# Performance work log

Hardware: AMD Instinct MI355X
Metric: run time of the kernel (lower is better)

## Reference

```python
import jax, jax.numpy as jnp
import numpy as np

EMBED_DIM = 768
N_HEADS = 12
HEAD_DIM = EMBED_DIM // N_HEADS


def setup_inputs() -> dict:
    key = jax.random.key(0)
    ks = jax.random.split(key, 5)
    s = 1.0 / np.sqrt(EMBED_DIM)
    x = jax.random.normal(ks[0], (8, 1024, EMBED_DIM), dtype=jnp.float32)
    w_qkv = jax.random.normal(ks[1], (EMBED_DIM, 3 * EMBED_DIM), dtype=jnp.float32) * s
    b_qkv = jnp.zeros((3 * EMBED_DIM,), dtype=jnp.float32)
    w_proj = jax.random.normal(ks[2], (EMBED_DIM, EMBED_DIM), dtype=jnp.float32) * s
    b_proj = jnp.zeros((EMBED_DIM,), dtype=jnp.float32)
    return {"x": x, "w_qkv": w_qkv, "b_qkv": b_qkv, "w_proj": w_proj, "b_proj": b_proj}


def reference(x, w_qkv, b_qkv, w_proj, b_proj):
    B, S, D = x.shape
    H, Hd = N_HEADS, HEAD_DIM
    qkv = x @ w_qkv + b_qkv                      # [B,S,3D]
    qkv = qkv.reshape(B, S, 3, H, Hd).transpose(2, 0, 3, 1, 4)  # [3,B,H,S,Hd]
    q, k, v = qkv[0], qkv[1], qkv[2]
    scale = Hd ** -0.5
    attn = jnp.einsum('bhqd,bhkd->bhqk', q, k) * scale  # [B,H,S,S]
    attn = jax.nn.softmax(attn, axis=-1)
    out = jnp.einsum('bhqk,bhkd->bhqd', attn, v)        # [B,H,S,Hd]
    out = out.transpose(0, 2, 1, 3).reshape(B, S, D)
    return out @ w_proj + b_proj
```

## Files before the change

kernel.cpp:

```cpp
#include <hip/hip_runtime.h>
#include <stdint.h>

typedef unsigned short ushort_t;
typedef __bf16 bf16x8 __attribute__((ext_vector_type(8)));
typedef float floatx4 __attribute__((ext_vector_type(4)));

#define B_   8
#define S_   1024
#define D_   768
#define H_   12
#define M_   (B_ * S_)
#define N3_  (3 * D_)
#define QK_  1536

static __device__ __forceinline__ void gl_lds16(const void* g, void* l) {
  __builtin_amdgcn_global_load_lds((const __attribute__((address_space(1))) void*)g,
                                   (__attribute__((address_space(3))) void*)l,
                                   16, 0, 0);
}

static __device__ __forceinline__ ushort_t f2bf(float f) {
  __bf16 h = (__bf16)f;
  return __builtin_bit_cast(unsigned short, h);
}

static __device__ __forceinline__ void store_out(ushort_t* p, float v) { *p = f2bf(v); }
static __device__ __forceinline__ void store_out(float* p, float v) { *p = v; }

static __device__ __forceinline__ void transpose_tile(const float* __restrict__ W,
                                                      ushort_t* __restrict__ Wt,
                                                      int K, int N, int bx, int by,
                                                      int t) {
  __shared__ float tile[32][33];
  const int n0 = bx * 32, k0 = by * 32;
  const int tx = t & 31, ty = t >> 5;
#pragma unroll
  for (int i = 0; i < 4; ++i)
    tile[ty + i * 8][tx] = W[(size_t)(k0 + ty + i * 8) * N + n0 + tx];
  __syncthreads();
#pragma unroll
  for (int i = 0; i < 4; ++i)
    Wt[(size_t)(n0 + ty + i * 8) * K + k0 + tx] = f2bf(tile[tx][ty + i * 8]);
}

__global__ __launch_bounds__(256) void prep_kernel(const float* __restrict__ x,
                                                   ushort_t* __restrict__ xb,
                                                   const float* __restrict__ w_qkv,
                                                   ushort_t* __restrict__ wqkvt,
                                                   const float* __restrict__ w_proj,
                                                   ushort_t* __restrict__ wprojt) {
  const int gb = blockIdx.x, t = threadIdx.x;
  if (gb < 24576) {
    const int i = gb * 256 + t;
    xb[i] = f2bf(x[i]);
  } else if (gb < 24576 + 1728) {
    const int lb = gb - 24576;
    transpose_tile(w_qkv, wqkvt, D_, N3_, lb % 72, lb / 72, t);
  } else {
    const int lb = gb - 24576 - 1728;
    transpose_tile(w_proj, wprojt, D_, D_, lb % 24, lb / 24, t);
  }
}

template <typename OutT, bool SPLITV>
__global__ __launch_bounds__(256, 4) void gemm128(const ushort_t* __restrict__ A,
                                                  const ushort_t* __restrict__ Bt,
                                                  const float* __restrict__ bias,
                                                  OutT* __restrict__ C, int CN,
                                                  ushort_t* __restrict__ vt,
                                                  int NBX, int CHUNK) {
  __shared__ __align__(16) ushort_t As[2][128 * 32];
  __shared__ __align__(16) ushort_t Bs[2][128 * 32];

  const int t = threadIdx.x;
  const int wave = t >> 6, lane = t & 63;
  const int quad = lane >> 4, l15 = lane & 15;
  const int wm = wave >> 1, wn = wave & 1;

  const int g = blockIdx.x;
  const int swz = (g & 7) * CHUNK + (g >> 3);
  const int bx = swz % NBX, by = swz / NBX;
  const int m0 = by * 128, n0 = bx * 128;

  const int rsub = wave * 16 + (lane >> 2);
  const int scol = ((lane & 3) ^ ((lane >> 2) & 3)) * 8;

  const int slotq = (quad ^ (l15 & 3)) * 8;

  const int arow = wm * 64 + l15;
  const int brow = wn * 64 + l15;

  const ushort_t* At  = A + (size_t)m0 * 768;
  const ushort_t* Bte = Bt + (size_t)n0 * 768;

  floatx4 acc[4][4];
#pragma unroll
  for (int i = 0; i < 4; ++i)
#pragma unroll
    for (int j = 0; j < 4; ++j) acc[i][j] = (floatx4)0.0f;

#pragma unroll
  for (int c = 0; c < 2; ++c) {
    gl_lds16(At + (size_t)(c * 64 + rsub) * 768 + scol,
             &As[0][(c * 64 + wave * 16) * 32]);
    gl_lds16(Bte + (size_t)(c * 64 + rsub) * 768 + scol,
             &Bs[0][(c * 64 + wave * 16) * 32]);
  }
  asm volatile("s_waitcnt vmcnt(0)" ::: "memory");
  __builtin_amdgcn_s_barrier();

#pragma unroll 2
  for (int kt = 0; kt < 24; ++kt) {
    const ushort_t* Ab = As[kt & 1];
    const ushort_t* Bb = Bs[kt & 1];

    if (kt + 1 < 24) {
      const int k1 = (kt + 1) * 32;
      ushort_t* An = As[(kt + 1) & 1];
      ushort_t* Bn = Bs[(kt + 1) & 1];
#pragma unroll
      for (int c = 0; c < 2; ++c) {
        gl_lds16(At + (size_t)(c * 64 + rsub) * 768 + k1 + scol,
                 An + (c * 64 + wave * 16) * 32);
        gl_lds16(Bte + (size_t)(c * 64 + rsub) * 768 + k1 + scol,
                 Bn + (c * 64 + wave * 16) * 32);
      }
    }

    bf16x8 af[4], bfr[4];
#pragma unroll
    for (int mi = 0; mi < 4; ++mi)
      af[mi] = *(const bf16x8*)(Ab + (arow + mi * 16) * 32 + slotq);
#pragma unroll
    for (int ni = 0; ni < 4; ++ni)
      bfr[ni] = *(const bf16x8*)(Bb + (brow + ni * 16) * 32 + slotq);
#pragma unroll
    for (int mi = 0; mi < 4; ++mi)
#pragma unroll
      for (int ni = 0; ni < 4; ++ni)
        acc[mi][ni] = __builtin_amdgcn_mfma_f32_16x16x32_bf16(af[mi], bfr[ni], acc[mi][ni], 0, 0, 0);

    asm volatile("s_waitcnt vmcnt(0)" ::: "memory");
    __builtin_amdgcn_s_barrier();
  }

#pragma unroll
  for (int ni = 0; ni < 4; ++ni) {
    const int colb = n0 + wn * 64 + ni * 16;
    const int col = colb + l15;
    const float bb = bias[col];
    if (SPLITV && colb >= 1536) {
      const int hh = (colb - 1536) >> 6;
      const int d  = ((colb - 1536) & 63) + l15;
      const int bh = (m0 >> 10) * H_ + hh;
      ushort_t* vrow = vt + ((size_t)bh * 64 + d) * 1024 +
                       (m0 & 1023) + wm * 64 + quad * 4;
#pragma unroll
      for (int mi = 0; mi < 4; ++mi) {
        ushort4 pk;
        pk.x = f2bf(acc[mi][ni][0] + bb);
        pk.y = f2bf(acc[mi][ni][1] + bb);
        pk.z = f2bf(acc[mi][ni][2] + bb);
        pk.w = f2bf(acc[mi][ni][3] + bb);
        *(ushort4*)(vrow + mi * 16) = pk;
      }
    } else {
#pragma unroll
      for (int mi = 0; mi < 4; ++mi) {
#pragma unroll
        for (int r = 0; r < 4; ++r) {
          const int row = m0 + wm * 64 + mi * 16 + quad * 4 + r;
          store_out(&C[(size_t)row * CN + col], acc[mi][ni][r] + bb);
        }
      }
    }
  }
}

__global__ __launch_bounds__(256) void attn_kernel(const ushort_t* __restrict__ qk,
                                                   const ushort_t* __restrict__ vt,
                                                   ushort_t* __restrict__ o) {
  __shared__ __align__(16) ushort_t Qs[128 * 64];
  __shared__ __align__(16) ushort_t Ks[64 * 64];
  __shared__ __align__(16) ushort_t Vts[64 * 64];
  __shared__ __align__(16) ushort_t Ps[128 * 72];

  const int t = threadIdx.x;
  const int wave = t >> 6, lane = t & 63;
  const int quad = lane >> 4, l15 = lane & 15;

  const int g = blockIdx.x;
  const int xcd = g & 7, gi = g >> 3;
  const int bh = xcd * 12 + (gi >> 3);
  const int q0 = (gi & 7) * 128;
  const int h = bh % H_;
  const int bS = (bh / H_) * S_;
  const ushort_t* vbase = vt + (size_t)bh * 64 * 1024;

#pragma unroll
  for (int c = 0; c < 4; ++c) {
    const int i0 = c * 256 + wave * 64;
    const int i = i0 + lane;
    const int row = i >> 3, sg = (i & 7) ^ (row & 7);
    gl_lds16(qk + (size_t)(bS + q0 + row) * QK_ + h * 64 + sg * 8, Qs + i0 * 8);
  }
  __syncthreads();

  bf16x8 qf[2][2];
#pragma unroll
  for (int mi = 0; mi < 2; ++mi)
#pragma unroll
    for (int kb = 0; kb < 2; ++kb)
      qf[mi][kb] = *(const bf16x8*)(Qs + (wave * 32 + mi * 16 + l15) * 64 +
                                    (((kb * 4 + quad) ^ (l15 & 7)) * 8));

  floatx4 oa[2][4];
#pragma unroll
  for (int mi = 0; mi < 2; ++mi)
#pragma unroll
    for (int d = 0; d < 4; ++d) oa[mi][d] = (floatx4)0.0f;
  float lsum[2][4] = {{0.f, 0.f, 0.f, 0.f}, {0.f, 0.f, 0.f, 0.f}};

  for (int kv0 = 0; kv0 < S_; kv0 += 64) {
#pragma unroll
    for (int c = 0; c < 2; ++c) {
      const int i0 = c * 256 + wave * 64;
      const int i = i0 + lane;
      const int row = i >> 3, sg = (i & 7) ^ (row & 7);
      gl_lds16(qk + (size_t)(bS + kv0 + row) * QK_ + 768 + h * 64 + sg * 8,
               Ks + i0 * 8);
      gl_lds16(vbase + (size_t)row * 1024 + kv0 + sg * 8, Vts + i0 * 8);
    }
    __syncthreads();

    floatx4 sa[2][4];
#pragma unroll
    for (int mi = 0; mi < 2; ++mi)
#pragma unroll
      for (int ni = 0; ni < 4; ++ni) sa[mi][ni] = (floatx4)0.0f;
#pragma unroll
    for (int ni = 0; ni < 4; ++ni)
#pragma unroll
      for (int kb = 0; kb < 2; ++kb) {
        const bf16x8 kf = *(const bf16x8*)(Ks + (ni * 16 + l15) * 64 +
                                           (((kb * 4 + quad) ^ (l15 & 7)) * 8));
#pragma unroll
        for (int mi = 0; mi < 2; ++mi)
          sa[mi][ni] = __builtin_amdgcn_mfma_f32_16x16x32_bf16(qf[mi][kb], kf, sa[mi][ni], 0, 0, 0);
      }

#pragma unroll
    for (int mi = 0; mi < 2; ++mi)
#pragma unroll
      for (int r = 0; r < 4; ++r) {
        float psum = 0.0f;
#pragma unroll
        for (int ni = 0; ni < 4; ++ni) {
          const float p = __expf(fmaf(sa[mi][ni][r], 0.125f, -16.0f));
          psum += p;
          Ps[(wave * 32 + mi * 16 + quad * 4 + r) * 72 + ni * 16 + l15] = f2bf(p);
        }
        lsum[mi][r] += psum;
      }

#pragma unroll
    for (int kb = 0; kb < 2; ++kb) {
      bf16x8 vf[4];
#pragma unroll
      for (int dt = 0; dt < 4; ++dt)
        vf[dt] = *(const bf16x8*)(Vts + (dt * 16 + l15) * 64 +
                                  (((kb * 4 + quad) ^ (l15 & 7)) * 8));
#pragma unroll
      for (int mi = 0; mi < 2; ++mi) {
        const bf16x8 pf = *(const bf16x8*)(Ps + (wave * 32 + mi * 16 + l15) * 72 +
                                           kb * 32 + quad * 8);
#pragma unroll
        for (int dt = 0; dt < 4; ++dt)
          oa[mi][dt] = __builtin_amdgcn_mfma_f32_16x16x32_bf16(pf, vf[dt], oa[mi][dt], 0, 0, 0);
      }
    }
    __syncthreads();
  }

#pragma unroll
  for (int mi = 0; mi < 2; ++mi)
#pragma unroll
    for (int r = 0; r < 4; ++r) {
#pragma unroll
      for (int off = 8; off >= 1; off >>= 1)
        lsum[mi][r] += __shfl_xor(lsum[mi][r], off, 64);
    }

#pragma unroll
  for (int mi = 0; mi < 2; ++mi)
#pragma unroll
    for (int dt = 0; dt < 4; ++dt)
#pragma unroll
      for (int r = 0; r < 4; ++r) {
        const int q = q0 + wave * 32 + mi * 16 + quad * 4 + r;
        o[(size_t)(bS + q) * D_ + h * 64 + dt * 16 + l15] =
            f2bf(oa[mi][dt][r] / lsum[mi][r]);
      }
}

extern "C" void kernel_launch(void* const* d_in, const int* in_sizes, int n_in,
                              void* d_out, int out_size, void* d_ws, size_t ws_size,
                              hipStream_t stream) {
  const float* x      = (const float*)d_in[0];
  const float* w_qkv  = (const float*)d_in[1];
  const float* b_qkv  = (const float*)d_in[2];
  const float* w_proj = (const float*)d_in[3];
  const float* b_proj = (const float*)d_in[4];
  float* out = (float*)d_out;

  ushort_t* xb = (ushort_t*)d_out;

  ushort_t* vtb    = (ushort_t*)d_ws;
  ushort_t* wqkvt  = vtb + (size_t)96 * 64 * 1024;
  ushort_t* wprojt = wqkvt + (size_t)N3_ * D_;
  ushort_t* qkb    = wprojt + (size_t)D_ * D_;
  ushort_t* attnb  = qkb + (size_t)M_ * QK_;

  prep_kernel<<<24576 + 1728 + 576, 256, 0, stream>>>(x, xb, w_qkv, wqkvt,
                                                      w_proj, wprojt);
  gemm128<ushort_t, true><<<1152, 256, 0, stream>>>(xb, wqkvt, b_qkv, qkb, QK_,
                                                    vtb, 18, 144);
  attn_kernel<<<dim3(768), 256, 0, stream>>>(qkb, vtb, attnb);
  gemm128<float, false><<<384, 256, 0, stream>>>(attnb, wprojt, b_proj, out, D_,
                                                 nullptr, 6, 48);
}
```

Before: 208.0 us.

## Load GEMM B operand directly from global into registers, bypassing LDS

The B tile in the 128x128 GEMM is no longer staged through shared memory. Each wave now loads its own B fragments straight from global memory into registers, double-buffered across k-steps. Only A goes through LDS via global_load_lds, and the A swizzle pattern is changed. This halves LDS traffic and footprint and could raise occupancy, but B is no longer shared between waves (the two wm waves both read it), so global and L2 traffic grows and register pressure rises.

```diff
diff --git a/kernel.cpp b/kernel.cpp
--- a/kernel.cpp
+++ b/kernel.cpp
@@ -70,7 +70,6 @@
                                                   ushort_t* __restrict__ vt,
                                                   int NBX, int CHUNK) {
   __shared__ __align__(16) ushort_t As[2][128 * 32];
-  __shared__ __align__(16) ushort_t Bs[2][128 * 32];
 
   const int t = threadIdx.x;
   const int wave = t >> 6, lane = t & 63;
@@ -83,15 +82,16 @@
   const int m0 = by * 128, n0 = bx * 128;
 
   const int rsub = wave * 16 + (lane >> 2);
-  const int scol = ((lane & 3) ^ ((lane >> 2) & 3)) * 8;
-
-  const int slotq = (quad ^ (l15 & 3)) * 8;
+  const int scol = ((lane & 3) ^ ((lane >> 3) & 3)) * 8;
+
+  const int slotq = (quad ^ ((l15 >> 1) & 3)) * 8;
 
   const int arow = wm * 64 + l15;
   const int brow = wn * 64 + l15;
 
   const ushort_t* At  = A + (size_t)m0 * 768;
   const ushort_t* Bte = Bt + (size_t)n0 * 768;
+  const ushort_t* Bl  = Bte + (size_t)brow * 768 + quad * 8;
 
   floatx4 acc[4][4];
 #pragma unroll
@@ -99,49 +99,67 @@
 #pragma unroll
     for (int j = 0; j < 4; ++j) acc[i][j] = (floatx4)0.0f;
 
-#pragma unroll
-  for (int c = 0; c < 2; ++c) {
+  bf16x8 b0[4], b1[4];
+#pragma unroll
+  for (int ni = 0; ni < 4; ++ni)
+    b0[ni] = *(const bf16x8*)(Bl + (size_t)(ni * 16) * 768);
+#pragma unroll
+  for (int c = 0; c < 2; ++c)
     gl_lds16(At + (size_t)(c * 64 + rsub) * 768 + scol,
              &As[0][(c * 64 + wave * 16) * 32]);
-    gl_lds16(Bte + (size_t)(c * 64 + rsub) * 768 + scol,
-             &Bs[0][(c * 64 + wave * 16) * 32]);
-  }
   asm volatile("s_waitcnt vmcnt(0)" ::: "memory");
   __builtin_amdgcn_s_barrier();
 
-#pragma unroll 2
-  for (int kt = 0; kt < 24; ++kt) {
-    const ushort_t* Ab = As[kt & 1];
-    const ushort_t* Bb = Bs[kt & 1];
-
-    if (kt + 1 < 24) {
-      const int k1 = (kt + 1) * 32;
-      ushort_t* An = As[(kt + 1) & 1];
-      ushort_t* Bn = Bs[(kt + 1) & 1];
-#pragma unroll
-      for (int c = 0; c < 2; ++c) {
-        gl_lds16(At + (size_t)(c * 64 + rsub) * 768 + k1 + scol,
-                 An + (c * 64 + wave * 16) * 32);
-        gl_lds16(Bte + (size_t)(c * 64 + rsub) * 768 + k1 + scol,
-                 Bn + (c * 64 + wave * 16) * 32);
-      }
-    }
-
-    bf16x8 af[4], bfr[4];
-#pragma unroll
-    for (int mi = 0; mi < 4; ++mi)
-      af[mi] = *(const bf16x8*)(Ab + (arow + mi * 16) * 32 + slotq);
-#pragma unroll
-    for (int ni = 0; ni < 4; ++ni)
-      bfr[ni] = *(const bf16x8*)(Bb + (brow + ni * 16) * 32 + slotq);
-#pragma unroll
-    for (int mi = 0; mi < 4; ++mi)
-#pragma unroll
-      for (int ni = 0; ni < 4; ++ni)
-        acc[mi][ni] = __builtin_amdgcn_mfma_f32_16x16x32_bf16(af[mi], bfr[ni], acc[mi][ni], 0, 0, 0);
-
-    asm volatile("s_waitcnt vmcnt(0)" ::: "memory");
-    __builtin_amdgcn_s_barrier();
+#pragma unroll 1
+  for (int kt = 0; kt < 24; kt += 2) {
+    {
+      const ushort_t* Ab = As[0];
+      if (kt + 1 < 24) {
+        const int k1 = (kt + 1) * 32;
+#pragma unroll
+        for (int ni = 0; ni < 4; ++ni)
+          b1[ni] = *(const bf16x8*)(Bl + (size_t)(ni * 16) * 768 + k1);
+#pragma unroll
+        for (int c = 0; c < 2; ++c)
+          gl_lds16(At + (size_t)(c * 64 + rsub) * 768 + k1 + scol,
+                   &As[1][(c * 64 + wave * 16) * 32]);
+      }
+      bf16x8 af[4];
+#pragma unroll
+      for (int mi = 0; mi < 4; ++mi)
+        af[mi] = *(const bf16x8*)(Ab + (arow + mi * 16) * 32 + slotq);
+#pragma unroll
+      for (int mi = 0; mi < 4; ++mi)
+#pragma unroll
+        for (int ni = 0; ni < 4; ++ni)
+          acc[mi][ni] = __builtin_amdgcn_mfma_f32_16x16x32_bf16(af[mi], b0[ni], acc[mi][ni], 0, 0, 0);
+      asm volatile("s_waitcnt vmcnt(0)" ::: "memory");
+      __builtin_amdgcn_s_barrier();
+    }
+    {
+      const ushort_t* Ab = As[1];
+      if (kt + 2 < 24) {
+        const int k2 = (kt + 2) * 32;
+#pragma unroll
+        for (int ni = 0; ni < 4; ++ni)
+          b0[ni] = *(const bf16x8*)(Bl + (size_t)(ni * 16) * 768 + k2);
+#pragma unroll
+        for (int c = 0; c < 2; ++c)
+          gl_lds16(At + (size_t)(c * 64 + rsub) * 768 + k2 + scol,
+                   &As[0][(c * 64 + wave * 16) * 32]);
+      }
+      bf16x8 af[4];
+#pragma unroll
+      for (int mi = 0; mi < 4; ++mi)
+        af[mi] = *(const bf16x8*)(Ab + (arow + mi * 16) * 32 + slotq);
+#pragma unroll
+      for (int mi = 0; mi < 4; ++mi)
+#pragma unroll
+        for (int ni = 0; ni < 4; ++ni)
+          acc[mi][ni] = __builtin_amdgcn_mfma_f32_16x16x32_bf16(af[mi], b1[ni], acc[mi][ni], 0, 0, 0);
+      asm volatile("s_waitcnt vmcnt(0)" ::: "memory");
+      __builtin_amdgcn_s_barrier();
+    }
   }
 
 #pragma unroll
```

Measured after the change: 246.4 us. +18.5%, slower.

## Fuse fp32-to-bf16 conversion of x into the QKV GEMM A-tile load

Applied to the files above, without the earlier changes.

Drops the separate pass that converts x to bf16. The QKV GEMM now reads fp32 x straight into registers, converts it and writes bf16 to LDS, with the next tile's loads issued before the MFMAs. This saves a full write and re-read of the activation and one large launch. In exchange, the A operand no longer uses direct global-to-LDS loads, it reads twice as many bytes per element, and it adds VGPR pressure. The LDS swizzle pattern also changes, and the loop now syncs with __syncthreads instead of an explicit waitcnt plus barrier.

```diff
diff --git a/kernel.cpp b/kernel.cpp
--- a/kernel.cpp
+++ b/kernel.cpp
@@ -43,27 +43,21 @@
     Wt[(size_t)(n0 + ty + i * 8) * K + k0 + tx] = f2bf(tile[tx][ty + i * 8]);
 }
 
-__global__ __launch_bounds__(256) void prep_kernel(const float* __restrict__ x,
-                                                   ushort_t* __restrict__ xb,
-                                                   const float* __restrict__ w_qkv,
+__global__ __launch_bounds__(256) void prep_kernel(const float* __restrict__ w_qkv,
                                                    ushort_t* __restrict__ wqkvt,
                                                    const float* __restrict__ w_proj,
                                                    ushort_t* __restrict__ wprojt) {
   const int gb = blockIdx.x, t = threadIdx.x;
-  if (gb < 24576) {
-    const int i = gb * 256 + t;
-    xb[i] = f2bf(x[i]);
-  } else if (gb < 24576 + 1728) {
-    const int lb = gb - 24576;
-    transpose_tile(w_qkv, wqkvt, D_, N3_, lb % 72, lb / 72, t);
+  if (gb < 1728) {
+    transpose_tile(w_qkv, wqkvt, D_, N3_, gb % 72, gb / 72, t);
   } else {
-    const int lb = gb - 24576 - 1728;
+    const int lb = gb - 1728;
     transpose_tile(w_proj, wprojt, D_, D_, lb % 24, lb / 24, t);
   }
 }
 
-template <typename OutT, bool SPLITV>
-__global__ __launch_bounds__(256, 4) void gemm128(const ushort_t* __restrict__ A,
+template <typename OutT, bool SPLITV, bool AF32>
+__global__ __launch_bounds__(256, 4) void gemm128(const void* __restrict__ Ap,
                                                   const ushort_t* __restrict__ Bt,
                                                   const float* __restrict__ bias,
                                                   OutT* __restrict__ C, int CN,
@@ -83,48 +77,87 @@
   const int m0 = by * 128, n0 = bx * 128;
 
   const int rsub = wave * 16 + (lane >> 2);
-  const int scol = ((lane & 3) ^ ((lane >> 2) & 3)) * 8;
-
-  const int slotq = (quad ^ (l15 & 3)) * 8;
+  const int scol = ((lane & 3) ^ ((lane >> 3) & 3)) * 8;
+
+  const int slotq = (quad ^ ((l15 >> 1) & 3)) * 8;
 
   const int arow = wm * 64 + l15;
   const int brow = wn * 64 + l15;
 
-  const ushort_t* At  = A + (size_t)m0 * 768;
+  const float*    Ax  = (const float*)Ap + (size_t)m0 * 768;
+  const ushort_t* At  = (const ushort_t*)Ap + (size_t)m0 * 768;
   const ushort_t* Bte = Bt + (size_t)n0 * 768;
 
+  const int xrow0 = wave * 16 + (lane >> 2);
+  const int xslot = (lane & 3) * 8;
+
   floatx4 acc[4][4];
 #pragma unroll
   for (int i = 0; i < 4; ++i)
 #pragma unroll
     for (int j = 0; j < 4; ++j) acc[i][j] = (floatx4)0.0f;
 
-#pragma unroll
-  for (int c = 0; c < 2; ++c) {
-    gl_lds16(At + (size_t)(c * 64 + rsub) * 768 + scol,
-             &As[0][(c * 64 + wave * 16) * 32]);
-    gl_lds16(Bte + (size_t)(c * 64 + rsub) * 768 + scol,
-             &Bs[0][(c * 64 + wave * 16) * 32]);
-  }
-  asm volatile("s_waitcnt vmcnt(0)" ::: "memory");
-  __builtin_amdgcn_s_barrier();
+  if (AF32) {
+    floatx4 xa[2][2];
+#pragma unroll
+    for (int it = 0; it < 2; ++it) {
+      const float* src = Ax + (size_t)(it * 64 + xrow0) * 768 + scol;
+      xa[it][0] = *(const floatx4*)(src);
+      xa[it][1] = *(const floatx4*)(src + 4);
+    }
+#pragma unroll
+    for (int c = 0; c < 2; ++c)
+      gl_lds16(Bte + (size_t)(c * 64 + rsub) * 768 + scol,
+               &Bs[0][(c * 64 + wave * 16) * 32]);
+#pragma unroll
+    for (int it = 0; it < 2; ++it) {
+      bf16x8 w;
+#pragma unroll
+      for (int j = 0; j < 4; ++j) {
+        w[j]     = (__bf16)xa[it][0][j];
+        w[4 + j] = (__bf16)xa[it][1][j];
+      }
+      *(bf16x8*)(&As[0][(it * 64 + xrow0) * 32 + xslot]) = w;
+    }
+  } else {
+#pragma unroll
+    for (int c = 0; c < 2; ++c) {
+      gl_lds16(At + (size_t)(c * 64 + rsub) * 768 + scol,
+               &As[0][(c * 64 + wave * 16) * 32]);
+      gl_lds16(Bte + (size_t)(c * 64 + rsub) * 768 + scol,
+               &Bs[0][(c * 64 + wave * 16) * 32]);
+    }
+  }
+  __syncthreads();
 
 #pragma unroll 2
   for (int kt = 0; kt < 24; ++kt) {
     const ushort_t* Ab = As[kt & 1];
     const ushort_t* Bb = Bs[kt & 1];
-
-    if (kt + 1 < 24) {
-      const int k1 = (kt + 1) * 32;
-      ushort_t* An = As[(kt + 1) & 1];
-      ushort_t* Bn = Bs[(kt + 1) & 1];
-#pragma unroll
-      for (int c = 0; c < 2; ++c) {
-        gl_lds16(At + (size_t)(c * 64 + rsub) * 768 + k1 + scol,
-                 An + (c * 64 + wave * 16) * 32);
+    const bool p1 = (kt + 1) < 24;
+    const int k1 = (kt + 1) * 32;
+    ushort_t* An = As[(kt + 1) & 1];
+    ushort_t* Bn = Bs[(kt + 1) & 1];
+
+    floatx4 xa[2][2];
+    if (p1) {
+      if (AF32) {
+#pragma unroll
+        for (int it = 0; it < 2; ++it) {
+          const float* src = Ax + (size_t)(it * 64 + xrow0) * 768 + k1 + scol;
+          xa[it][0] = *(const floatx4*)(src);
+          xa[it][1] = *(const floatx4*)(src + 4);
+        }
+      } else {
+#pragma unroll
+        for (int c = 0; c < 2; ++c)
+          gl_lds16(At + (size_t)(c * 64 + rsub) * 768 + k1 + scol,
+                   An + (c * 64 + wave * 16) * 32);
+      }
+#pragma unroll
+      for (int c = 0; c < 2; ++c)
         gl_lds16(Bte + (size_t)(c * 64 + rsub) * 768 + k1 + scol,
                  Bn + (c * 64 + wave * 16) * 32);
-      }
     }
 
     bf16x8 af[4], bfr[4];
@@ -140,8 +173,19 @@
       for (int ni = 0; ni < 4; ++ni)
         acc[mi][ni] = __builtin_amdgcn_mfma_f32_16x16x32_bf16(af[mi], bfr[ni], acc[mi][ni], 0, 0, 0);
 
-    asm volatile("s_waitcnt vmcnt(0)" ::: "memory");
-    __builtin_amdgcn_s_barrier();
+    if (AF32 && p1) {
+#pragma unroll
+      for (int it = 0; it < 2; ++it) {
+        bf16x8 w;
+#pragma unroll
+        for (int j = 0; j < 4; ++j) {
+          w[j]     = (__bf16)xa[it][0][j];
+          w[4 + j] = (__bf16)xa[it][1][j];
+        }
+        *(bf16x8*)(&An[(it * 64 + xrow0) * 32 + xslot]) = w;
+      }
+    }
+    __syncthreads();
   }
 
 #pragma unroll
@@ -313,19 +357,16 @@
   const float* b_proj = (const float*)d_in[4];
   float* out = (float*)d_out;
 
-  ushort_t* xb = (ushort_t*)d_out;
-
   ushort_t* vtb    = (ushort_t*)d_ws;
   ushort_t* wqkvt  = vtb + (size_t)96 * 64 * 1024;
   ushort_t* wprojt = wqkvt + (size_t)N3_ * D_;
   ushort_t* qkb    = wprojt + (size_t)D_ * D_;
   ushort_t* attnb  = qkb + (size_t)M_ * QK_;
 
-  prep_kernel<<<24576 + 1728 + 576, 256, 0, stream>>>(x, xb, w_qkv, wqkvt,
-                                                      w_proj, wprojt);
-  gemm128<ushort_t, true><<<1152, 256, 0, stream>>>(xb, wqkvt, b_qkv, qkb, QK_,
-                                                    vtb, 18, 144);
+  prep_kernel<<<1728 + 576, 256, 0, stream>>>(w_qkv, wqkvt, w_proj, wprojt);
+  gemm128<ushort_t, true, true><<<1152, 256, 0, stream>>>(x, wqkvt, b_qkv, qkb,
+                                                          QK_, vtb, 18, 144);
   attn_kernel<<<dim3(768), 256, 0, stream>>>(qkb, vtb, attnb);
-  gemm128<float, false><<<384, 256, 0, stream>>>(attnb, wprojt, b_proj, out, D_,
-                                                 nullptr, 6, 48);
-}
+  gemm128<float, false, false><<<384, 256, 0, stream>>>(attnb, wprojt, b_proj,
+                                                        out, D_, nullptr, 6, 48);
+}
```

Measured after the change: 200.6 us. -3.5%, faster.
